# Optimization experiments

Measured on AMD Instinct MI355X. Metric: run time of the kernel, lower is better.

The kernel has to match this reference:

```python
import jax, jax.numpy as jnp
import numpy as np

NEG_INF = -10000000000.0
HEADS = 16


def setup_inputs() -> dict:
    key = jax.random.key(0)
    ks = jax.random.split(key, 12)
    B, S, E = 2, 2048, 1024
    sc = 1.0 / np.sqrt(E)
    inp = {
        "input_queries": jax.random.normal(ks[0], (B, S, E), jnp.float32),
        "input_keys": jax.random.normal(ks[1], (B, S, E), jnp.float32),
        "input_values": jax.random.normal(ks[2], (B, S, E), jnp.float32),
        # causal mask: True where attention is disallowed (masked_fill where mask==True)
        "mask": jnp.triu(jnp.ones((S, S), jnp.bool_), k=1)[None, None],
        "Wq": jax.random.normal(ks[3], (E, E), jnp.float32) * sc,
        "bq": jax.random.normal(ks[4], (E,), jnp.float32) * 0.01,
        "Wk": jax.random.normal(ks[5], (E, E), jnp.float32) * sc,
        "bk": jax.random.normal(ks[6], (E,), jnp.float32) * 0.01,
        "Wv": jax.random.normal(ks[7], (E, E), jnp.float32) * sc,
        "bv": jax.random.normal(ks[8], (E,), jnp.float32) * 0.01,
        "Wo": jax.random.normal(ks[9], (E, E), jnp.float32) * sc,
        "bo": jax.random.normal(ks[10], (E,), jnp.float32) * 0.01,
    }
    return inp


def reference(input_queries, input_keys, input_values, mask, Wq, bq, Wk, bk, Wv, bv, Wo, bo):
    B, S, E = input_queries.shape
    H = HEADS
    D = E // H
    # torch Linear: y = x @ W.T + b
    q = (input_queries @ Wq.T + bq).reshape(B, S, H, D).transpose(0, 2, 1, 3)  # bhsd
    k = (input_keys @ Wk.T + bk).reshape(B, S, H, D).transpose(0, 2, 1, 3)
    v = (input_values @ Wv.T + bv).reshape(B, S, H, D).transpose(0, 2, 1, 3)
    scores = jnp.einsum('bhqd,bhkd->bhqk', q, k) / jnp.sqrt(jnp.asarray(D, q.dtype))
    scores = jnp.where(mask, jnp.asarray(NEG_INF, scores.dtype), scores)
    attn = jax.nn.softmax(scores, axis=-1)
    out = jnp.einsum('bhqk,bhkd->bhqd', attn, v).transpose(0, 2, 1, 3).reshape(B, S, E)
    return out @ Wo.T + bo
```

## Files before the change

### kernel.cpp

```cpp
#include <hip/hip_runtime.h>
#include <hip/hip_bf16.h>

#define DEVI __device__ __forceinline__

using bf16x8 = __attribute__((ext_vector_type(8))) short;
using f32x4  = __attribute__((ext_vector_type(4))) float;

DEVI unsigned short f2bf(float f){
  unsigned int u = __float_as_uint(f);
  return (unsigned short)((u + 0x7fffu + ((u>>16)&1u)) >> 16);
}

DEVI unsigned int cvt_pk_bf16(float lo, float hi){
  unsigned int r;
  asm("v_cvt_pk_bf16_f32 %0, %1, %2" : "=v"(r) : "v"(lo), "v"(hi));
  return r;
}

DEVI void gload_lds16(const unsigned short* src, unsigned short* lds){
  __builtin_amdgcn_global_load_lds((const __attribute__((address_space(1))) void*)src,
                                   (__attribute__((address_space(3))) void*)lds, 16, 0, 0);
}

__global__ __launch_bounds__(256) void convert_kernel(
  const float* __restrict__ Xq, const float* __restrict__ Xk, const float* __restrict__ Xv,
  const float* __restrict__ Wq, const float* __restrict__ Wk, const float* __restrict__ Wv,
  const float* __restrict__ Wo, unsigned short* __restrict__ ws)
{
  const int y = blockIdx.y;
  const float* src;
  unsigned short* dst;
  int n4;
  if (y < 3){
    src = (y==0)?Xq:((y==1)?Xk:Xv);
    dst = ws + (size_t)y*4194304;
    n4 = 1048576;
  } else {
    src = (y==3)?Wq:((y==4)?Wk:((y==5)?Wv:Wo));
    dst = ws + 12582912 + (size_t)(y-3)*1048576;
    n4 = 262144;
  }
  const int stride = gridDim.x * 256;
  for (int i = blockIdx.x*256 + threadIdx.x; i < n4; i += stride){
    float4 v = ((const float4*)src)[i];
    uint2 u;
    u.x = cvt_pk_bf16(v.x, v.y);
    u.y = cvt_pk_bf16(v.z, v.w);
    ((uint2*)dst)[i] = u;
  }
}

__global__ __launch_bounds__(256) void proj_qkv_kernel(
  const unsigned short* __restrict__ Xb, const unsigned short* __restrict__ Wb,
  const float* __restrict__ Bq, const float* __restrict__ Bk, const float* __restrict__ Bv,
  unsigned short* __restrict__ Qo, unsigned short* __restrict__ Ko, unsigned short* __restrict__ Vo)
{
  const int p = blockIdx.y;
  const unsigned short* __restrict__ A = Xb + (size_t)p*4194304;
  const unsigned short* __restrict__ B = Wb + (size_t)p*1048576;
  const float* __restrict__ Bb = (p==0)?Bq:((p==1)?Bk:Bv);
  unsigned short* __restrict__ Out = (p==0)?Qo:((p==1)?Ko:Vo);
  const float oscale = (p==0)?0.125f:1.0f;

  const int tm = blockIdx.x >> 3, tn = blockIdx.x & 7;
  const int m0 = tm*128, n0 = tn*128;
  const int tid = threadIdx.x;
  const int w = tid>>6, l = tid&63;
  const int wr = w>>1, wc = w&1;
  const int lg = l>>4, lr = l&15;

  __shared__ unsigned short As[128*64];
  __shared__ unsigned short Bs[128*64];

  f32x4 acc[4][4];
  #pragma unroll
  for (int i=0;i<4;i++)
    #pragma unroll
    for (int j=0;j<4;j++){ f32x4 z = {0.f,0.f,0.f,0.f}; acc[i][j] = z; }

  for (int kt=0; kt<1024; kt+=64){
    #pragma unroll
    for (int i=0;i<4;i++){
      int rbase = w*32 + i*8;
      gload_lds16(A + (size_t)(m0 + rbase + (l>>3))*1024 + kt + (l&7)*8, As + rbase*64);
      gload_lds16(B + (size_t)(n0 + rbase + (l>>3))*1024 + kt + (l&7)*8, Bs + rbase*64);
    }
    __syncthreads();

    #pragma unroll
    for (int ck=0;ck<2;ck++){
      bf16x8 af[4], bfr[4];
      #pragma unroll
      for (int f=0;f<4;f++){
        af[f]  = *(const bf16x8*)(As + (wr*64 + f*16 + lr)*64 + ck*32 + lg*8);
        bfr[f] = *(const bf16x8*)(Bs + (wc*64 + f*16 + lr)*64 + ck*32 + lg*8);
      }
      #pragma unroll
      for (int fr=0;fr<4;fr++)
        #pragma unroll
        for (int fc=0;fc<4;fc++)
          acc[fr][fc] = __builtin_amdgcn_mfma_f32_16x16x32_bf16(af[fr], bfr[fc], acc[fr][fc], 0,0,0);
    }
    __syncthreads();
  }

  #pragma unroll
  for (int fc=0;fc<4;fc++){
    int n = n0 + wc*64 + fc*16 + lr;
    float bias = Bb[n];
    int h = n>>6, d = n&63;
    #pragma unroll
    for (int fr=0;fr<4;fr++){
      #pragma unroll
      for (int r=0;r<4;r++){
        int m = m0 + wr*64 + fr*16 + lg*4 + r;
        int b = m>>11, s = m & 2047;
        float v = (acc[fr][fc][r] + bias) * oscale;
        Out[ ((size_t)((b<<4)+h)*2048 + (size_t)s)*64 + d ] = f2bf(v);
      }
    }
  }
}

__global__ __launch_bounds__(256) void attn_kernel(
  const unsigned short* __restrict__ Q, const unsigned short* __restrict__ Kb,
  const unsigned short* __restrict__ V, unsigned short* __restrict__ AO)
{
  const int idx = blockIdx.x;
  const int qt = 15 - (idx >> 5);
  const int bh = idx & 31;
  const size_t base = (size_t)bh * (2048*64);
  const int q0 = qt * 128;
  const int tid = threadIdx.x, w = tid>>6, l = tid&63;
  const int lg = l>>4, lr = l&15;

  __shared__ unsigned short Ks[64*64];
  __shared__ unsigned short Vs[64*64];
  __shared__ unsigned short Ps[4*32*64];
  unsigned short* Pw = Ps + w*2048;

  bf16x8 qf[2][2];
  #pragma unroll
  for (int qh=0; qh<2; qh++){
    const unsigned short* qp = Q + base + (size_t)(q0 + w*32 + qh*16 + lr)*64 + lg*8;
    qf[qh][0] = *(const bf16x8*)qp;
    qf[qh][1] = *(const bf16x8*)(qp + 32);
  }

  float m_i[2], l_i[2];
  f32x4 o_acc[2][4];
  #pragma unroll
  for (int qh=0;qh<2;qh++){
    m_i[qh] = -INFINITY; l_i[qh] = 0.f;
    #pragma unroll
    for (int dt=0;dt<4;dt++){ f32x4 z={0.f,0.f,0.f,0.f}; o_acc[qh][dt]=z; }
  }

  const int NT = 2*qt + 2;
  for (int kt=0; kt<NT; kt++){
    const int kv0 = kt*64;
    #pragma unroll
    for (int i=0;i<2;i++){
      int c = tid + i*256;
      int row = c>>3, kc = c&7;
      bf16x8 kv = *(const bf16x8*)(Kb + base + (size_t)(kv0+row)*64 + kc*8);
      *(bf16x8*)((char*)Ks + row*128 + ((kc*16) ^ ((row&7)<<4))) = kv;
    }
    #pragma unroll
    for (int i=0;i<2;i++){
      int d0 = w*8 + i*32;
      bf16x8 vv = *(const bf16x8*)(V + base + (size_t)(kv0+l)*64 + d0);
      #pragma unroll
      for (int j=0;j<8;j++){
        int dr = d0 + j;
        *(unsigned short*)((char*)Vs + dr*128 + ((l*2) ^ ((dr&7)<<4))) = (unsigned short)vv[j];
      }
    }
    __syncthreads();

    bf16x8 kf[4][2];
    #pragma unroll
    for (int t=0;t<4;t++){
      int rk = t*16 + lr;
      #pragma unroll
      for (int ck=0;ck<2;ck++)
        kf[t][ck] = *(const bf16x8*)((const char*)Ks + rk*128 + ((ck*64 + lg*16) ^ ((rk&7)<<4)));
    }

    #pragma unroll
    for (int qh=0; qh<2; qh++){
      f32x4 sacc[4];
      #pragma unroll
      for (int t=0;t<4;t++){ f32x4 z={0.f,0.f,0.f,0.f}; sacc[t]=z; }
      #pragma unroll
      for (int t=0;t<4;t++){
        sacc[t] = __builtin_amdgcn_mfma_f32_16x16x32_bf16(kf[t][0], qf[qh][0], sacc[t], 0,0,0);
        sacc[t] = __builtin_amdgcn_mfma_f32_16x16x32_bf16(kf[t][1], qf[qh][1], sacc[t], 0,0,0);
      }
      const int qq = q0 + w*32 + qh*16 + lr;
      if (kv0 + 63 > q0 + w*32 + qh*16){
        #pragma unroll
        for (int t=0;t<4;t++)
          #pragma unroll
          for (int r=0;r<4;r++){
            int kvv = kv0 + t*16 + lg*4 + r;
            if (kvv > qq) sacc[t][r] = -1e30f;
          }
      }
      float mt = sacc[0][0];
      #pragma unroll
      for (int t=0;t<4;t++)
        #pragma unroll
        for (int r=0;r<4;r++) mt = fmaxf(mt, sacc[t][r]);
      mt = fmaxf(mt, __shfl_xor(mt, 16));
      mt = fmaxf(mt, __shfl_xor(mt, 32));
      float mn = fmaxf(m_i[qh], mt);
      float sc = __expf(m_i[qh] - mn);
      m_i[qh] = mn;
      float rs = 0.f;
      #pragma unroll
      for (int t=0;t<4;t++)
        #pragma unroll
        for (int r=0;r<4;r++){
          float pv = __expf(sacc[t][r] - mn);
          sacc[t][r] = pv;
          rs += pv;
        }
      rs += __shfl_xor(rs, 16);
      rs += __shfl_xor(rs, 32);
      l_i[qh] = l_i[qh]*sc + rs;
      #pragma unroll
      for (int dt=0;dt<4;dt++)
        #pragma unroll
        for (int r=0;r<4;r++) o_acc[qh][dt][r] *= sc;

      const int prow = qh*16 + lr;
      char* pbase = (char*)Pw + prow*128;
      const int swz = (prow&7)<<4;
      #pragma unroll
      for (int t=0;t<4;t++){
        unsigned int u01 = cvt_pk_bf16(sacc[t][0], sacc[t][1]);
        unsigned int u23 = cvt_pk_bf16(sacc[t][2], sacc[t][3]);
        *(unsigned int*)(pbase + ((32*t + 8*lg    ) ^ swz)) = u01;
        *(unsigned int*)(pbase + ((32*t + 8*lg + 4) ^ swz)) = u23;
      }
    }

    bf16x8 vt[4][2];
    #pragma unroll
    for (int dt=0;dt<4;dt++){
      int rv = dt*16 + lr;
      #pragma unroll
      for (int ck=0;ck<2;ck++)
        vt[dt][ck] = *(const bf16x8*)((const char*)Vs + rv*128 + ((ck*64 + lg*16) ^ ((rv&7)<<4)));
    }
    #pragma unroll
    for (int qh=0; qh<2; qh++){
      const int prow = qh*16 + lr;
      const int swz = (prow&7)<<4;
      #pragma unroll
      for (int ck=0;ck<2;ck++){
        bf16x8 pb = *(const bf16x8*)((const char*)Pw + prow*128 + ((ck*64 + lg*16) ^ swz));
        #pragma unroll
        for (int dt=0;dt<4;dt++)
          o_acc[qh][dt] = __builtin_amdgcn_mfma_f32_16x16x32_bf16(vt[dt][ck], pb, o_acc[qh][dt], 0,0,0);
      }
    }
    __syncthreads();
  }

  const int b = bh>>4, h = bh&15;
  #pragma unroll
  for (int qh=0;qh<2;qh++){
    float inv = 1.0f / l_i[qh];
    int q = q0 + w*32 + qh*16 + lr;
    #pragma unroll
    for (int dt=0;dt<4;dt++){
      uint2 u;
      u.x = cvt_pk_bf16(o_acc[qh][dt][0]*inv, o_acc[qh][dt][1]*inv);
      u.y = cvt_pk_bf16(o_acc[qh][dt][2]*inv, o_acc[qh][dt][3]*inv);
      *(uint2*)(AO + ((size_t)b*2048 + q)*1024 + h*64 + dt*16 + lg*4) = u;
    }
  }
}

__global__ __launch_bounds__(256) void proj_out_kernel(
  const unsigned short* __restrict__ A, const unsigned short* __restrict__ B,
  const float* __restrict__ Bb, float* __restrict__ Out)
{
  const int tm = blockIdx.x >> 3, tn = blockIdx.x & 7;
  const int m0 = tm*128, n0 = tn*128;
  const int tid = threadIdx.x;
  const int w = tid>>6, l = tid&63;
  const int wr = w>>1, wc = w&1;
  const int lg = l>>4, lr = l&15;

  __shared__ unsigned short As[128*64];
  __shared__ unsigned short Bs[128*64];

  f32x4 acc[4][4];
  #pragma unroll
  for (int i=0;i<4;i++)
    #pragma unroll
    for (int j=0;j<4;j++){ f32x4 z = {0.f,0.f,0.f,0.f}; acc[i][j] = z; }

  for (int kt=0; kt<1024; kt+=64){
    #pragma unroll
    for (int i=0;i<4;i++){
      int rbase = w*32 + i*8;
      gload_lds16(A + (size_t)(m0 + rbase + (l>>3))*1024 + kt + (l&7)*8, As + rbase*64);
      gload_lds16(B + (size_t)(n0 + rbase + (l>>3))*1024 + kt + (l&7)*8, Bs + rbase*64);
    }
    __syncthreads();

    #pragma unroll
    for (int ck=0;ck<2;ck++){
      bf16x8 af[4], bfr[4];
      #pragma unroll
      for (int f=0;f<4;f++){
        af[f]  = *(const bf16x8*)(As + (wr*64 + f*16 + lr)*64 + ck*32 + lg*8);
        bfr[f] = *(const bf16x8*)(Bs + (wc*64 + f*16 + lr)*64 + ck*32 + lg*8);
      }
      #pragma unroll
      for (int fr=0;fr<4;fr++)
        #pragma unroll
        for (int fc=0;fc<4;fc++)
          acc[fr][fc] = __builtin_amdgcn_mfma_f32_16x16x32_bf16(af[fr], bfr[fc], acc[fr][fc], 0,0,0);
    }
    __syncthreads();
  }

  #pragma unroll
  for (int fc=0;fc<4;fc++){
    int n = n0 + wc*64 + fc*16 + lr;
    float bias = Bb[n];
    #pragma unroll
    for (int fr=0;fr<4;fr++){
      #pragma unroll
      for (int r=0;r<4;r++){
        int m = m0 + wr*64 + fr*16 + lg*4 + r;
        Out[(size_t)m*1024 + n] = acc[fr][fc][r] + bias;
      }
    }
  }
}

extern "C" void kernel_launch(void* const* d_in, const int* in_sizes, int n_in,
                              void* d_out, int out_size, void* d_ws, size_t ws_size,
                              hipStream_t stream)
{
  const float* Xq = (const float*)d_in[0];
  const float* Xk = (const float*)d_in[1];
  const float* Xv = (const float*)d_in[2];
  const float* Wq = (const float*)d_in[4];
  const float* bq = (const float*)d_in[5];
  const float* Wk = (const float*)d_in[6];
  const float* bk = (const float*)d_in[7];
  const float* Wv = (const float*)d_in[8];
  const float* bv = (const float*)d_in[9];
  const float* Wo = (const float*)d_in[10];
  const float* bo = (const float*)d_in[11];

  unsigned short* ws  = (unsigned short*)d_ws;
  unsigned short* Xb  = ws;
  unsigned short* Wb  = ws + 12582912;
  unsigned short* Qw  = ws + 16777216;
  unsigned short* Kw  = ws + 20971520;
  unsigned short* Vw  = ws + 25165824;
  unsigned short* AOw = ws + 29360128;
  float* out = (float*)d_out;

  convert_kernel<<<dim3(512,7), 256, 0, stream>>>(Xq,Xk,Xv,Wq,Wk,Wv,Wo, ws);
  proj_qkv_kernel<<<dim3(256,3), 256, 0, stream>>>(Xb, Wb, bq,bk,bv, Qw,Kw,Vw);
  attn_kernel<<<512, 256, 0, stream>>>(Qw,Kw,Vw,AOw);
  proj_out_kernel<<<256, 256, 0, stream>>>(AOw, Wb + 3*1048576, bo, out);
}
```

Measured before the change: 263.0 us.

## Restructure attention with 32x32 MFMA, async double-buffered K/V, register P, lazy rescale

Measured after the change: 254.7 us. 3.1% less time.

```diff
diff --git a/kernel.cpp b/kernel.cpp
--- a/kernel.cpp
+++ b/kernel.cpp
@@ -5,6 +5,9 @@
 
 using bf16x8 = __attribute__((ext_vector_type(8))) short;
 using f32x4  = __attribute__((ext_vector_type(4))) float;
+using f32x16 = __attribute__((ext_vector_type(16))) float;
+
+#define LOG2E 1.4426950408889634f
 
 DEVI unsigned short f2bf(float f){
   unsigned int u = __float_as_uint(f);
@@ -17,9 +20,21 @@
   return r;
 }
 
+#if __has_builtin(__builtin_amdgcn_exp2f)
+#define EXP2(x) __builtin_amdgcn_exp2f(x)
+#else
+#define EXP2(x) exp2f(x)
+#endif
+
 DEVI void gload_lds16(const unsigned short* src, unsigned short* lds){
   __builtin_amdgcn_global_load_lds((const __attribute__((address_space(1))) void*)src,
                                    (__attribute__((address_space(3))) void*)lds, 16, 0, 0);
+}
+
+DEVI bf16x8 mk8(unsigned w0, unsigned w1, unsigned w2, unsigned w3){
+  union { unsigned u[4]; bf16x8 v; } x;
+  x.u[0]=w0; x.u[1]=w1; x.u[2]=w2; x.u[3]=w3;
+  return x.v;
 }
 
 __global__ __launch_bounds__(256) void convert_kernel(
@@ -60,7 +75,7 @@
   const unsigned short* __restrict__ B = Wb + (size_t)p*1048576;
   const float* __restrict__ Bb = (p==0)?Bq:((p==1)?Bk:Bv);
   unsigned short* __restrict__ Out = (p==0)?Qo:((p==1)?Ko:Vo);
-  const float oscale = (p==0)?0.125f:1.0f;
+  const float oscale = (p==0)?(0.125f*LOG2E):1.0f;
 
   const int tm = blockIdx.x >> 3, tn = blockIdx.x & 7;
   const int m0 = tm*128, n0 = tn*128;
@@ -104,182 +119,221 @@
     __syncthreads();
   }
 
-  #pragma unroll
-  for (int fc=0;fc<4;fc++){
-    int n = n0 + wc*64 + fc*16 + lr;
-    float bias = Bb[n];
-    int h = n>>6, d = n&63;
-    #pragma unroll
-    for (int fr=0;fr<4;fr++){
-      #pragma unroll
-      for (int r=0;r<4;r++){
-        int m = m0 + wr*64 + fr*16 + lg*4 + r;
+  if (p == 2){
+    #pragma unroll
+    for (int fc=0;fc<4;fc++){
+      int n = n0 + wc*64 + fc*16 + lr;
+      float bias = Bb[n];
+      int h = n>>6, d = n&63;
+      #pragma unroll
+      for (int fr=0;fr<4;fr++){
+        int m = m0 + wr*64 + fr*16 + lg*4;
         int b = m>>11, s = m & 2047;
-        float v = (acc[fr][fc][r] + bias) * oscale;
-        Out[ ((size_t)((b<<4)+h)*2048 + (size_t)s)*64 + d ] = f2bf(v);
-      }
-    }
-  }
-}
-
-__global__ __launch_bounds__(256) void attn_kernel(
-  const unsigned short* __restrict__ Q, const unsigned short* __restrict__ Kb,
-  const unsigned short* __restrict__ V, unsigned short* __restrict__ AO)
+        uint2 u;
+        u.x = cvt_pk_bf16(acc[fr][fc][0]+bias, acc[fr][fc][1]+bias);
+        u.y = cvt_pk_bf16(acc[fr][fc][2]+bias, acc[fr][fc][3]+bias);
+        *(uint2*)(Out + (((size_t)((b<<4)+h)*64 + d)*2048 + s)) = u;
+      }
+    }
+  } else {
+    #pragma unroll
+    for (int fc=0;fc<4;fc++){
+      int n = n0 + wc*64 + fc*16 + lr;
+      float bias = Bb[n];
+      int h = n>>6, d = n&63;
+      #pragma unroll
+      for (int fr=0;fr<4;fr++){
+        #pragma unroll
+        for (int r=0;r<4;r++){
+          int m = m0 + wr*64 + fr*16 + lg*4 + r;
+          int b = m>>11, s = m & 2047;
+          float v = (acc[fr][fc][r] + bias) * oscale;
+          Out[ ((size_t)((b<<4)+h)*2048 + (size_t)s)*64 + d ] = f2bf(v);
+        }
+      }
+    }
+  }
+}
+
+__global__ __launch_bounds__(256,2) void attn_kernel(
+  const unsigned short* __restrict__ Q, const unsigned short* __restrict__ Kg,
+  const unsigned short* __restrict__ Vt, unsigned short* __restrict__ AO)
 {
   const int idx = blockIdx.x;
   const int qt = 15 - (idx >> 5);
   const int bh = idx & 31;
-  const size_t base = (size_t)bh * (2048*64);
+  const size_t base = (size_t)bh * 131072;
   const int q0 = qt * 128;
   const int tid = threadIdx.x, w = tid>>6, l = tid&63;
-  const int lg = l>>4, lr = l&15;
-
-  __shared__ unsigned short Ks[64*64];
-  __shared__ unsigned short Vs[64*64];
-  __shared__ unsigned short Ps[4*32*64];
-  unsigned short* Pw = Ps + w*2048;
-
-  bf16x8 qf[2][2];
+  const int lq = l & 31, hi = l >> 5;
+  const int qq = q0 + w*32 + lq;
+
+  __shared__ unsigned short Ks[2][4096];
+  __shared__ unsigned short Vs[2][4096];
+
+  bf16x8 qf[4];
+  {
+    const unsigned short* qp = Q + base + (size_t)qq*64;
+    #pragma unroll
+    for (int s=0;s<4;s++) qf[s] = *(const bf16x8*)(qp + s*16 + hi*8);
+  }
+
+  f32x16 oacc[2];
   #pragma unroll
-  for (int qh=0; qh<2; qh++){
-    const unsigned short* qp = Q + base + (size_t)(q0 + w*32 + qh*16 + lr)*64 + lg*8;
-    qf[qh][0] = *(const bf16x8*)qp;
-    qf[qh][1] = *(const bf16x8*)(qp + 32);
-  }
-
-  float m_i[2], l_i[2];
-  f32x4 o_acc[2][4];
-  #pragma unroll
-  for (int qh=0;qh<2;qh++){
-    m_i[qh] = -INFINITY; l_i[qh] = 0.f;
-    #pragma unroll
-    for (int dt=0;dt<4;dt++){ f32x4 z={0.f,0.f,0.f,0.f}; o_acc[qh][dt]=z; }
-  }
+  for (int dt=0;dt<2;dt++)
+    #pragma unroll
+    for (int r=0;r<16;r++) oacc[dt][r] = 0.f;
+  float m_i = -INFINITY, l_i = 0.f;
 
   const int NT = 2*qt + 2;
-  for (int kt=0; kt<NT; kt++){
+
+  auto stage = [&](int kt, int half){
     const int kv0 = kt*64;
     #pragma unroll
     for (int i=0;i<2;i++){
       int c = tid + i*256;
-      int row = c>>3, kc = c&7;
-      bf16x8 kv = *(const bf16x8*)(Kb + base + (size_t)(kv0+row)*64 + kc*8);
-      *(bf16x8*)((char*)Ks + row*128 + ((kc*16) ^ ((row&7)<<4))) = kv;
-    }
-    #pragma unroll
-    for (int i=0;i<2;i++){
-      int d0 = w*8 + i*32;
-      bf16x8 vv = *(const bf16x8*)(V + base + (size_t)(kv0+l)*64 + d0);
-      #pragma unroll
-      for (int j=0;j<8;j++){
-        int dr = d0 + j;
-        *(unsigned short*)((char*)Vs + dr*128 + ((l*2) ^ ((dr&7)<<4))) = (unsigned short)vv[j];
-      }
-    }
+      int row = c>>3;
+      int kc = (c&7) ^ (row&7);
+      gload_lds16(Kg + base + (size_t)(kv0+row)*64 + kc*8, &Ks[half][0] + c*8);
+      gload_lds16(Vt + base + (size_t)row*2048 + kv0 + kc*8, &Vs[half][0] + c*8);
+    }
+  };
+
+  stage(0, 0);
+  __syncthreads();
+
+  for (int kt=0; kt<NT; kt++){
+    const int cur = kt & 1;
+    if (kt+1 < NT) stage(kt+1, cur^1);
+    const int kv0 = kt*64;
+
+    f32x16 sacc[2];
+    #pragma unroll
+    for (int kvt=0;kvt<2;kvt++)
+      #pragma unroll
+      for (int r=0;r<16;r++) sacc[kvt][r] = 0.f;
+
+    __builtin_amdgcn_s_setprio(1);
+    #pragma unroll
+    for (int kvt=0;kvt<2;kvt++){
+      int row = kvt*32 + lq;
+      const char* kb = (const char*)&Ks[cur][0] + row*128;
+      int swz = (row&7)<<4;
+      #pragma unroll
+      for (int s=0;s<4;s++){
+        bf16x8 kf = *(const bf16x8*)(kb + ((s*32 + hi*16) ^ swz));
+        sacc[kvt] = __builtin_amdgcn_mfma_f32_32x32x16_bf16(kf, qf[s], sacc[kvt], 0,0,0);
+      }
+    }
+    __builtin_amdgcn_s_setprio(0);
+
+    #pragma unroll
+    for (int kvt=0;kvt<2;kvt++){
+      if (kv0 + kvt*32 + 31 > q0 + w*32){
+        #pragma unroll
+        for (int r=0;r<16;r++){
+          int kvv = kv0 + kvt*32 + (r&3) + 8*(r>>2) + 4*hi;
+          if (kvv > qq) sacc[kvt][r] = -1e30f;
+        }
+      }
+    }
+
+    float mt = sacc[0][0];
+    #pragma unroll
+    for (int kvt=0;kvt<2;kvt++)
+      #pragma unroll
+      for (int r=0;r<16;r++) mt = fmaxf(mt, sacc[kvt][r]);
+    mt = fmaxf(mt, __shfl_xor(mt, 32));
+
+    if (__any(mt > m_i + 8.f)){
+      float mn = fmaxf(m_i, mt);
+      float sc = EXP2(m_i - mn);
+      m_i = mn;
+      l_i *= sc;
+      #pragma unroll
+      for (int dt=0;dt<2;dt++)
+        #pragma unroll
+        for (int r=0;r<16;r++) oacc[dt][r] *= sc;
+    }
+    float rs = 0.f;
+    #pragma unroll
+    for (int kvt=0;kvt<2;kvt++)
+      #pragma unroll
+      for (int r=0;r<16;r++){
+        float pv = EXP2(sacc[kvt][r] - m_i);
+        sacc[kvt][r] = pv;
+        rs += pv;
+      }
+    rs += __shfl_xor(rs, 32);
+    l_i += rs;
+
+    unsigned pa[8], pb[8], sa[8], sb[8];
+    #pragma unroll
+    for (int g=0; g<8; g++){
+      int kvt = g>>2, gl = g&3;
+      pa[g] = cvt_pk_bf16(sacc[kvt][4*gl+0], sacc[kvt][4*gl+1]);
+      pb[g] = cvt_pk_bf16(sacc[kvt][4*gl+2], sacc[kvt][4*gl+3]);
+      sa[g] = __shfl_xor(pa[g], 32);
+      sb[g] = __shfl_xor(pb[g], 32);
+    }
+    bf16x8 pfrag[4];
+    #pragma unroll
+    for (int s=0;s<4;s++){
+      int g0 = (s>>1)*4 + 2*(s&1);
+      unsigned w0 = hi ? sa[g0+1] : pa[g0];
+      unsigned w1 = hi ? sb[g0+1] : pb[g0];
+      unsigned w2 = hi ? pa[g0+1] : sa[g0];
+      unsigned w3 = hi ? pb[g0+1] : sb[g0];
+      pfrag[s] = mk8(w0, w1, w2, w3);
+    }
+
+    __builtin_amdgcn_s_setprio(1);
+    #pragma unroll
+    for (int dt=0;dt<2;dt++){
+      int row = dt*32 + lq;
+      const char* vb = (const char*)&Vs[cur][0] + row*128;
+      int swz = (row&7)<<4;
+      #pragma unroll
+      for (int s=0;s<4;s++){
+        bf16x8 vf = *(const bf16x8*)(vb + ((s*32 + hi*16) ^ swz));
+        oacc[dt] = __builtin_amdgcn_mfma_f32_32x32x16_bf16(vf, pfrag[s], oacc[dt], 0,0,0);
+      }
+    }
+    __builtin_amdgcn_s_setprio(0);
+
     __syncthreads();
-
-    bf16x8 kf[4][2];
-    #pragma unroll
-    for (int t=0;t<4;t++){
-      int rk = t*16 + lr;
-      #pragma unroll
-      for (int ck=0;ck<2;ck++)
-        kf[t][ck] = *(const bf16x8*)((const char*)Ks + rk*128 + ((ck*64 + lg*16) ^ ((rk&7)<<4)));
-    }
-
-    #pragma unroll
-    for (int qh=0; qh<2; qh++){
-      f32x4 sacc[4];
-      #pragma unroll
-      for (int t=0;t<4;t++){ f32x4 z={0.f,0.f,0.f,0.f}; sacc[t]=z; }
-      #pragma unroll
-      for (int t=0;t<4;t++){
-        sacc[t] = __builtin_amdgcn_mfma_f32_16x16x32_bf16(kf[t][0], qf[qh][0], sacc[t], 0,0,0);
-        sacc[t] = __builtin_amdgcn_mfma_f32_16x16x32_bf16(kf[t][1], qf[qh][1], sacc[t], 0,0,0);
-      }
-      const int qq = q0 + w*32 + qh*16 + lr;
-      if (kv0 + 63 > q0 + w*32 + qh*16){
-        #pragma unroll
-        for (int t=0;t<4;t++)
-          #pragma unroll
-          for (int r=0;r<4;r++){
-            int kvv = kv0 + t*16 + lg*4 + r;
-            if (kvv > qq) sacc[t][r] = -1e30f;
-          }
-      }
-      float mt = sacc[0][0];
-      #pragma unroll
-      for (int t=0;t<4;t++)
-        #pragma unroll
-        for (int r=0;r<4;r++) mt = fmaxf(mt, sacc[t][r]);
-      mt = fmaxf(mt, __shfl_xor(mt, 16));
-      mt = fmaxf(mt, __shfl_xor(mt, 32));
-      float mn = fmaxf(m_i[qh], mt);
-      float sc = __expf(m_i[qh] - mn);
-      m_i[qh] = mn;
-      float rs = 0.f;
-      #pragma unroll
-      for (int t=0;t<4;t++)
-        #pragma unroll
-        for (int r=0;r<4;r++){
-          float pv = __expf(sacc[t][r] - mn);
-          sacc[t][r] = pv;
-          rs += pv;
-        }
-      rs += __shfl_xor(rs, 16);
-      rs += __shfl_xor(rs, 32);
-      l_i[qh] = l_i[qh]*sc + rs;
-      #pragma unroll
-      for (int dt=0;dt<4;dt++)
-        #pragma unroll
-        for (int r=0;r<4;r++) o_acc[qh][dt][r] *= sc;
-
-      const int prow = qh*16 + lr;
-      char* pbase = (char*)Pw + prow*128;
-      const int swz = (prow&7)<<4;
-      #pragma unroll
-      for (int t=0;t<4;t++){
-        unsigned int u01 = cvt_pk_bf16(sacc[t][0], sacc[t][1]);
-        unsigned int u23 = cvt_pk_bf16(sacc[t][2], sacc[t][3]);
-        *(unsigned int*)(pbase + ((32*t + 8*lg    ) ^ swz)) = u01;
-        *(unsigned int*)(pbase + ((32*t + 8*lg + 4) ^ swz)) = u23;
-      }
-    }
-
-    bf16x8 vt[4][2];
-    #pragma unroll
-    for (int dt=0;dt<4;dt++){
-      int rv = dt*16 + lr;
-      #pragma unroll
-      for (int ck=0;ck<2;ck++)
-        vt[dt][ck] = *(const bf16x8*)((const char*)Vs + rv*128 + ((ck*64 + lg*16) ^ ((rv&7)<<4)));
-    }
-    #pragma unroll
-    for (int qh=0; qh<2; qh++){
-      const int prow = qh*16 + lr;
-      const int swz = (prow&7)<<4;
-      #pragma unroll
-      for (int ck=0;ck<2;ck++){
-        bf16x8 pb = *(const bf16x8*)((const char*)Pw + prow*128 + ((ck*64 + lg*16) ^ swz));
-        #pragma unroll
-        for (int dt=0;dt<4;dt++)
-          o_acc[qh][dt] = __builtin_amdgcn_mfma_f32_16x16x32_bf16(vt[dt][ck], pb, o_acc[qh][dt], 0,0,0);
-      }
-    }
-    __syncthreads();
-  }
-
+  }
+
+  unsigned short* Es = &Ks[0][0] + w*2048;
+  float inv = 1.0f / l_i;
+  {
+    char* eb = (char*)Es + lq*128;
+    int swz = (lq&7)<<4;
+    #pragma unroll
+    for (int dt=0;dt<2;dt++)
+      #pragma unroll
+      for (int g=0;g<4;g++){
+        int d0 = dt*32 + 8*g + 4*hi;
+        unsigned u0 = cvt_pk_bf16(oacc[dt][4*g+0]*inv, oacc[dt][4*g+1]*inv);
+        unsigned u1 = cvt_pk_bf16(oacc[dt][4*g+2]*inv, oacc[dt][4*g+3]*inv);
+        *(unsigned*)(eb + ((d0*2    ) ^ swz)) = u0;
+        *(unsigned*)(eb + ((d0*2 + 4) ^ swz)) = u1;
+      }
+  }
   const int b = bh>>4, h = bh&15;
-  #pragma unroll
-  for (int qh=0;qh<2;qh++){
-    float inv = 1.0f / l_i[qh];
-    int q = q0 + w*32 + qh*16 + lr;
-    #pragma unroll
-    for (int dt=0;dt<4;dt++){
-      uint2 u;
-      u.x = cvt_pk_bf16(o_acc[qh][dt][0]*inv, o_acc[qh][dt][1]*inv);
-      u.y = cvt_pk_bf16(o_acc[qh][dt][2]*inv, o_acc[qh][dt][3]*inv);
-      *(uint2*)(AO + ((size_t)b*2048 + q)*1024 + h*64 + dt*16 + lg*4) = u;
+  {
+    const char* rb = (const char*)Es + lq*128;
+    int swz = (lq&7)<<4;
+    unsigned short* op = AO + ((size_t)b*2048 + (q0 + w*32 + lq))*1024 + h*64 + hi*32;
+    #pragma unroll
+    for (int j=0;j<2;j++){
+      bf16x8 v = *(const bf16x8*)(rb + ((hi*64 + j*16) ^ swz));
+      *(bf16x8*)(op + j*8) = v;
+    }
+    #pragma unroll
+    for (int j=2;j<4;j++){
+      bf16x8 v = *(const bf16x8*)(rb + ((hi*64 + j*16) ^ swz));
+      *(bf16x8*)(op + j*8) = v;
     }
   }
 }
```
